# Kernel tuning notes

Hardware: AMD Instinct MI355X
Metric: run time of the kernel (lower is better)

## Reference

```python
import jax, jax.numpy as jnp
import numpy as np

D_MODEL, H, D_FF = 1024, 16, 4096
D_K = D_MODEL // H

def _linear_params(key, fan_in, fan_out):
    kw, kb = jax.random.split(key)
    lim = 1.0 / np.sqrt(fan_in)
    W = jax.random.uniform(kw, (fan_in, fan_out), minval=-lim, maxval=lim, dtype=jnp.float32)
    b = jax.random.uniform(kb, (fan_out,), minval=-lim, maxval=lim, dtype=jnp.float32)
    return W, b

def setup_inputs() -> dict:
    key = jax.random.key(0)
    ks = jax.random.split(key, 8)
    x = jax.random.normal(ks[0], (4, 2048, D_MODEL), dtype=jnp.float32)
    Wq, bq = _linear_params(ks[1], D_MODEL, D_MODEL)
    Wk, bk = _linear_params(ks[2], D_MODEL, D_MODEL)
    Wv, bv = _linear_params(ks[3], D_MODEL, D_MODEL)
    Wo, bo = _linear_params(ks[4], D_MODEL, D_MODEL)
    W1, b1 = _linear_params(ks[5], D_MODEL, D_FF)
    W2, b2 = _linear_params(ks[6], D_FF, D_MODEL)
    g1 = jnp.ones((D_MODEL,), jnp.float32); be1 = jnp.zeros((D_MODEL,), jnp.float32)
    g2 = jnp.ones((D_MODEL,), jnp.float32); be2 = jnp.zeros((D_MODEL,), jnp.float32)
    return {"x": x, "Wq": Wq, "bq": bq, "Wk": Wk, "bk": bk, "Wv": Wv, "bv": bv,
            "Wo": Wo, "bo": bo, "W1": W1, "b1": b1, "W2": W2, "b2": b2,
            "g1": g1, "be1": be1, "g2": g2, "be2": be2}

def _layernorm(x, g, b, eps=1e-5):
    mu = jnp.mean(x, axis=-1, keepdims=True)
    var = jnp.mean(jnp.square(x - mu), axis=-1, keepdims=True)
    return (x - mu) * jax.lax.rsqrt(var + eps) * g + b

def reference(x, Wq, bq, Wk, bk, Wv, bv, Wo, bo, W1, b1, W2, b2, g1, be1, g2, be2):
    B, S, _ = x.shape
    # project and split heads: [B, H, S, D_K]
    q = (x @ Wq + bq).reshape(B, S, H, D_K).transpose(0, 2, 1, 3)
    k = (x @ Wk + bk).reshape(B, S, H, D_K).transpose(0, 2, 1, 3)
    v = (x @ Wv + bv).reshape(B, S, H, D_K).transpose(0, 2, 1, 3)
    scores = jnp.einsum('bhqd,bhkd->bhqk', q, k) / np.sqrt(D_K).astype(np.float32)
    attn = jax.nn.softmax(scores, axis=-1)
    out = jnp.einsum('bhqk,bhkd->bhqd', attn, v)
    out = out.transpose(0, 2, 1, 3).reshape(B, S, D_MODEL)
    attn_out = out @ Wo + bo
    x1 = _layernorm(x + attn_out, g1, be1)
    ffn = jax.nn.relu(x1 @ W1 + b1) @ W2 + b2  # dropout is identity in eval
    return _layernorm(x1 + ffn, g2, be2)
```

## Files before the change

kernel.cpp:

```cpp
#include <hip/hip_runtime.h>

typedef __bf16 bf16;
typedef __bf16 bf16x4 __attribute__((ext_vector_type(4)));
typedef __bf16 bf16x8 __attribute__((ext_vector_type(8)));
typedef float  f32x4  __attribute__((ext_vector_type(4)));

#define DM   1024
#define NH   16
#define DKH  64
#define DFF  4096
#define SEQL 2048
#define NTOK 8192

typedef __attribute__((address_space(1))) void GAS;
typedef __attribute__((address_space(3))) void LAS;

__device__ inline void gload_lds16(const void* g, void* l) {
    __builtin_amdgcn_global_load_lds((GAS*)g, (LAS*)l, 16, 0, 0);
}

__global__ void cast_f32_bf16(const float* __restrict__ in, bf16* __restrict__ out, long n) {
    long i = ((long)blockIdx.x * 256 + threadIdx.x) * 4;
    long stride = (long)gridDim.x * 256 * 4;
    for (; i < n; i += stride) {
        float4 v = *(const float4*)(in + i);
        bf16x4 o = {(bf16)v.x, (bf16)v.y, (bf16)v.z, (bf16)v.w};
        *(bf16x4*)(out + i) = o;
    }
}

__global__ void transpose_cast(const float* __restrict__ src, bf16* __restrict__ dst, int R, int C) {
    __shared__ float t[32][33];
    int c0 = blockIdx.x * 32, r0 = blockIdx.y * 32;
    int tx = threadIdx.x, ty = threadIdx.y;
#pragma unroll
    for (int i = 0; i < 4; ++i)
        t[ty + i * 8][tx] = src[(long)(r0 + ty + i * 8) * C + c0 + tx];
    __syncthreads();
#pragma unroll
    for (int i = 0; i < 4; ++i)
        dst[(long)(c0 + ty + i * 8) * R + r0 + tx] = (bf16)t[tx][ty + i * 8];
}

__global__ void concat3(const float* __restrict__ a, const float* __restrict__ b,
                        const float* __restrict__ c, float* __restrict__ out) {
    int i = blockIdx.x * 256 + threadIdx.x;
    if (i < 1024) out[i] = a[i];
    else if (i < 2048) out[i] = b[i - 1024];
    else if (i < 3072) out[i] = c[i - 2048];
}

__global__ void build_vt(const bf16* __restrict__ qkv, bf16* __restrict__ vt) {
    __shared__ bf16 t[32][33];
    int bh = blockIdx.z, b = bh >> 4, h = bh & 15;
    int s0 = blockIdx.x * 32, d0 = blockIdx.y * 32;
    int tx = threadIdx.x, ty = threadIdx.y;
#pragma unroll
    for (int i = 0; i < 4; ++i)
        t[ty + i * 8][tx] = qkv[(long)(b * SEQL + s0 + ty + i * 8) * 3072 + 2 * DM + h * DKH + d0 + tx];
    __syncthreads();
#pragma unroll
    for (int i = 0; i < 4; ++i)
        vt[((long)bh * DKH + d0 + ty + i * 8) * SEQL + s0 + tx] = (bf16)t[tx][ty + i * 8];
}

__global__ __launch_bounds__(512, 2)
void gemm8p(const bf16* __restrict__ A, const bf16* __restrict__ Bt,
            const float* __restrict__ bias,
            float* __restrict__ Cf, bf16* __restrict__ Ch,
            int N, int lda, int Klen, int relu, long strideCf) {
    __shared__ bf16 As[4][4][256][8];
    __shared__ bf16 Bs[4][4][256][8];
    const int tid = threadIdx.x;
    const int lane = tid & 63;
    const int wv = tid >> 6;
    const int wr = wv >> 2, wc = wv & 3;
    const int lr = lane & 15, lg = lane >> 4;

    unsigned gx = gridDim.x, gy = gridDim.y;
    unsigned nwg = gx * gy * gridDim.z;
    unsigned wg = (blockIdx.z * gy + blockIdx.y) * gx + blockIdx.x;
    unsigned swz = (wg & 7) * (nwg >> 3) + (wg >> 3);
    unsigned bxi = swz % gx;
    unsigned rem = swz / gx;
    unsigned byi = rem % gy, bzi = rem / gy;

    const long brow = (long)byi * 256;
    const long bcol = (long)bxi * 256;
    const bf16* Ap = A + (long)bzi * Klen;
    const bf16* Bp = Bt + (long)bzi * Klen;
    float* Cfp = Cf ? Cf + (long)bzi * strideCf : nullptr;
    const float* biasp = (bzi == 0) ? bias : nullptr;

    auto stageA = [&](int X) {
        const int kt = X * 32, buf = X & 3;
#pragma unroll
        for (int j = 0; j < 2; ++j) {
            int l = j * 512 + tid;
            int kg = l >> 8, row = l & 255;
            gload_lds16(Ap + (brow + row) * (long)lda + kt + kg * 8, &As[buf][kg][row][0]);
        }
    };
    auto stageB = [&](int X) {
        const int kt = X * 32, buf = X & 3;
#pragma unroll
        for (int j = 0; j < 2; ++j) {
            int l = j * 512 + tid;
            int kg = l >> 8, row = l & 255;
            gload_lds16(Bp + (bcol + row) * (long)lda + kt + kg * 8, &Bs[buf][kg][row][0]);
        }
    };

    const int NT = Klen / 32;
    f32x4 acc[8][4] = {};

    for (int p = 0; p < 3 && p < NT; ++p) { stageA(p); stageB(p); }

    for (int T = 0; T < NT; ++T) {
        const int cur = T & 3;
        if (T + 3 < NT) stageA(T + 3);
        if (T + 3 < NT)      asm volatile("s_waitcnt vmcnt(10)" ::: "memory");
        else if (T + 2 < NT) asm volatile("s_waitcnt vmcnt(8)"  ::: "memory");
        else if (T + 1 < NT) asm volatile("s_waitcnt vmcnt(4)"  ::: "memory");
        else                 asm volatile("s_waitcnt vmcnt(0)"  ::: "memory");
        __builtin_amdgcn_s_barrier();
        asm volatile("" ::: "memory");

        bf16x8 bfv[4], af[4];
#pragma unroll
        for (int n = 0; n < 4; ++n)
            bfv[n] = *(const bf16x8*)(&Bs[cur][lg][wc * 64 + n * 16 + lr][0]);
#pragma unroll
        for (int m = 0; m < 4; ++m)
            af[m] = *(const bf16x8*)(&As[cur][lg][wr * 128 + m * 16 + lr][0]);
        asm volatile("s_waitcnt lgkmcnt(0)" ::: "memory");
        __builtin_amdgcn_sched_barrier(0);
        __builtin_amdgcn_s_setprio(1);
#pragma unroll
        for (int m = 0; m < 4; ++m)
#pragma unroll
            for (int n = 0; n < 4; ++n)
                acc[m][n] = __builtin_amdgcn_mfma_f32_16x16x32_bf16(af[m], bfv[n], acc[m][n], 0, 0, 0);
        __builtin_amdgcn_s_setprio(0);

        bf16x8 af2[4];
#pragma unroll
        for (int m = 0; m < 4; ++m)
            af2[m] = *(const bf16x8*)(&As[cur][lg][wr * 128 + (4 + m) * 16 + lr][0]);
        if (T + 3 < NT) stageB(T + 3);
        asm volatile("" ::: "memory");
        __builtin_amdgcn_s_barrier();
        asm volatile("s_waitcnt lgkmcnt(0)" ::: "memory");
        __builtin_amdgcn_sched_barrier(0);
        __builtin_amdgcn_s_setprio(1);
#pragma unroll
        for (int m = 0; m < 4; ++m)
#pragma unroll
            for (int n = 0; n < 4; ++n)
                acc[4 + m][n] = __builtin_amdgcn_mfma_f32_16x16x32_bf16(af2[m], bfv[n], acc[4 + m][n], 0, 0, 0);
        __builtin_amdgcn_s_setprio(0);
        asm volatile("" ::: "memory");
        __builtin_amdgcn_s_barrier();
    }

#pragma unroll
    for (int m = 0; m < 8; ++m) {
#pragma unroll
        for (int n = 0; n < 4; ++n) {
            long gcol = bcol + wc * 64 + n * 16 + lr;
            float bv = biasp ? biasp[gcol] : 0.f;
#pragma unroll
            for (int r = 0; r < 4; ++r) {
                long grow = brow + wr * 128 + m * 16 + lg * 4 + r;
                float v = acc[m][n][r] + bv;
                if (relu) v = v > 0.f ? v : 0.f;
                if (Cfp) Cfp[grow * N + gcol] = v;
                if (Ch) Ch[grow * N + gcol] = (bf16)v;
            }
        }
    }
}

__global__ __launch_bounds__(256, 3)
void attn_fwd(const bf16* __restrict__ qkv, const bf16* __restrict__ vt,
              bf16* __restrict__ attn_o) {
    __shared__ bf16 Ks[2][64][64];
    __shared__ bf16 Vs[2][64][64];
    __shared__ bf16 Plds[4][16][64];
    const int tid = threadIdx.x, lane = tid & 63, w = tid >> 6;
    const int lr = lane & 15, lg = lane >> 4;

    unsigned nwg = gridDim.x * gridDim.y;
    unsigned wg = blockIdx.y * gridDim.x + blockIdx.x;
    unsigned cpx = nwg >> 3;
    unsigned swzid = (wg & 7) * cpx + (wg >> 3);
    const int bx = swzid % gridDim.x, bh = swzid / gridDim.x;
    const int b = bh >> 4, h = bh & 15;
    const int q0 = bx * 128 + w * 32;

    const bf16* Q  = qkv + (long)b * SEQL * 3072 + h * DKH;
    const bf16* Kp = qkv + (long)b * SEQL * 3072 + DM + h * DKH;
    const bf16* Vp = vt + (long)bh * DKH * SEQL;

    const int r0 = w * 8 + (lane >> 3);
    const int cbb = ((lane & 7) * 16) ^ ((r0 & 7) << 4);
    const int cb = cbb >> 1;

    auto stage = [&](int buf, int j0) {
#pragma unroll
        for (int c = 0; c < 2; ++c) {
            bf16* kd = &Ks[buf][0][0] + c * 2048 + w * 512 + lane * 8;
            bf16* vd = &Vs[buf][0][0] + c * 2048 + w * 512 + lane * 8;
            gload_lds16(Kp + (long)(j0 + c * 32 + r0) * 3072 + cb, kd);
            gload_lds16(Vp + (long)(c * 32 + r0) * SEQL + j0 + cb, vd);
        }
    };

    stage(0, 0);

    bf16x8 aq[2][2];
#pragma unroll
    for (int a = 0; a < 2; ++a)
#pragma unroll
        for (int kh = 0; kh < 2; ++kh) {
            bf16x8 q = *(const bf16x8*)(Q + (long)(q0 + a * 16 + lr) * 3072 + kh * 32 + lg * 8);
#pragma unroll
            for (int e = 0; e < 8; ++e) q[e] = (bf16)((float)q[e] * 0.125f);
            aq[a][kh] = q;
        }

    float mrow[2] = {-1e30f, -1e30f};
    float lrow[2] = {0.f, 0.f};
    f32x4 accO[2][4] = {};
    char* pbase = (char*)&Plds[w][0][0];
    const int psw = (lr & 7) << 4;
    const f32x4 zero = {0.f, 0.f, 0.f, 0.f};
    int cur = 0;

    for (int it = 0; it < SEQL / 64; ++it) {
        if (it < SEQL / 64 - 1) {
            stage(cur ^ 1, (it + 1) * 64);
            asm volatile("s_waitcnt vmcnt(4)" ::: "memory");
        } else {
            asm volatile("s_waitcnt vmcnt(0)" ::: "memory");
        }
        __builtin_amdgcn_s_barrier();
        asm volatile("" ::: "memory");

        const char* Kbuf = (const char*)&Ks[cur][0][0];
        const char* Vbuf = (const char*)&Vs[cur][0][0];

        bf16x8 kf[4][2];
#pragma unroll
        for (int jh = 0; jh < 4; ++jh) {
            int row = jh * 16 + lr;
            int sw = (row & 7) << 4;
            kf[jh][0] = *(const bf16x8*)(Kbuf + row * 128 + ((lg * 16) ^ sw));
            kf[jh][1] = *(const bf16x8*)(Kbuf + row * 128 + ((64 + lg * 16) ^ sw));
        }
        bf16x8 vf[4][2];
#pragma unroll
        for (int c = 0; c < 4; ++c) {
            int row = c * 16 + lr;
            int sw = (row & 7) << 4;
            vf[c][0] = *(const bf16x8*)(Vbuf + row * 128 + ((lg * 16) ^ sw));
            vf[c][1] = *(const bf16x8*)(Vbuf + row * 128 + ((64 + lg * 16) ^ sw));
        }

#pragma unroll
        for (int a = 0; a < 2; ++a) {
            f32x4 s[4];
#pragma unroll
            for (int jh = 0; jh < 4; ++jh) {
                f32x4 t = __builtin_amdgcn_mfma_f32_16x16x32_bf16(kf[jh][0], aq[a][0], zero, 0, 0, 0);
                s[jh] = __builtin_amdgcn_mfma_f32_16x16x32_bf16(kf[jh][1], aq[a][1], t, 0, 0, 0);
            }
            float pm = s[0][0];
#pragma unroll
            for (int jh = 0; jh < 4; ++jh)
#pragma unroll
                for (int r = 0; r < 4; ++r) pm = fmaxf(pm, s[jh][r]);
            pm = fmaxf(pm, __shfl_xor(pm, 16));
            pm = fmaxf(pm, __shfl_xor(pm, 32));
            float mnew = fmaxf(mrow[a], pm);
            float al = __expf(mrow[a] - mnew);
            mrow[a] = mnew;
            float psum = 0.f;
#pragma unroll
            for (int jh = 0; jh < 4; ++jh)
#pragma unroll
                for (int r = 0; r < 4; ++r) {
                    float p = __expf(s[jh][r] - mnew);
                    s[jh][r] = p;
                    psum += p;
                }
            psum += __shfl_xor(psum, 16);
            psum += __shfl_xor(psum, 32);
            lrow[a] = lrow[a] * al + psum;
#pragma unroll
            for (int jh = 0; jh < 4; ++jh) {
                bf16x4 pw = {(bf16)s[jh][0], (bf16)s[jh][1], (bf16)s[jh][2], (bf16)s[jh][3]};
                *(bf16x4*)(pbase + lr * 128 + ((jh * 32 + lg * 8) ^ psw)) = pw;
            }
            float alr[4];
#pragma unroll
            for (int r = 0; r < 4; ++r)
                alr[r] = __shfl(al, (lane & 48) | (lg * 4 + r));
#pragma unroll
            for (int c = 0; c < 4; ++c)
#pragma unroll
                for (int r = 0; r < 4; ++r) accO[a][c][r] *= alr[r];
            bf16x8 pa[2];
#pragma unroll
            for (int i = 0; i < 2; ++i)
                pa[i] = *(const bf16x8*)(pbase + lr * 128 + ((i * 64 + lg * 16) ^ psw));
#pragma unroll
            for (int c = 0; c < 4; ++c) {
                accO[a][c] = __builtin_amdgcn_mfma_f32_16x16x32_bf16(pa[0], vf[c][0], accO[a][c], 0, 0, 0);
                accO[a][c] = __builtin_amdgcn_mfma_f32_16x16x32_bf16(pa[1], vf[c][1], accO[a][c], 0, 0, 0);
            }
        }
        asm volatile("" ::: "memory");
        __builtin_amdgcn_s_barrier();
        cur ^= 1;
    }

#pragma unroll
    for (int a = 0; a < 2; ++a) {
        float linv = 1.0f / lrow[a];
        float invr[4];
#pragma unroll
        for (int r = 0; r < 4; ++r)
            invr[r] = __shfl(linv, (lane & 48) | (lg * 4 + r));
#pragma unroll
        for (int r = 0; r < 4; ++r) {
            long grow = (long)b * SEQL + q0 + a * 16 + lg * 4 + r;
#pragma unroll
            for (int c = 0; c < 4; ++c)
                attn_o[grow * DM + h * DKH + c * 16 + lr] = (bf16)(accO[a][c][r] * invr[r]);
        }
    }
}

__global__ __launch_bounds__(256)
void add_ln(const float* __restrict__ A, const float* __restrict__ B,
            const float* __restrict__ B2,
            const float* __restrict__ g, const float* __restrict__ be,
            float* __restrict__ outf, bf16* __restrict__ outh) {
    const int w = threadIdx.x >> 6, lane = threadIdx.x & 63;
    const long row = (long)blockIdx.x * 4 + w;
    const float4* pa = (const float4*)(A + row * DM);
    const float4* pb = (const float4*)(B + row * DM);
    const float4* pb2 = B2 ? (const float4*)(B2 + row * DM) : nullptr;
    float4 v[4];
    float s = 0.f;
#pragma unroll
    for (int i = 0; i < 4; ++i) {
        float4 a = pa[i * 64 + lane], bb = pb[i * 64 + lane];
        v[i] = make_float4(a.x + bb.x, a.y + bb.y, a.z + bb.z, a.w + bb.w);
        if (pb2) {
            float4 b2 = pb2[i * 64 + lane];
            v[i].x += b2.x; v[i].y += b2.y; v[i].z += b2.z; v[i].w += b2.w;
        }
        s += v[i].x + v[i].y + v[i].z + v[i].w;
    }
#pragma unroll
    for (int off = 32; off; off >>= 1) s += __shfl_xor(s, off);
    float mu = s * (1.0f / 1024.0f);
    float var = 0.f;
#pragma unroll
    for (int i = 0; i < 4; ++i) {
        float dx = v[i].x - mu, dy = v[i].y - mu, dz = v[i].z - mu, dw = v[i].w - mu;
        var += dx * dx + dy * dy + dz * dz + dw * dw;
    }
#pragma unroll
    for (int off = 32; off; off >>= 1) var += __shfl_xor(var, off);
    float rs = 1.0f / sqrtf(var * (1.0f / 1024.0f) + 1e-5f);
    const float4* pg = (const float4*)g;
    const float4* pe = (const float4*)be;
#pragma unroll
    for (int i = 0; i < 4; ++i) {
        float4 gg = pg[i * 64 + lane], ee = pe[i * 64 + lane];
        float4 o = make_float4((v[i].x - mu) * rs * gg.x + ee.x,
                               (v[i].y - mu) * rs * gg.y + ee.y,
                               (v[i].z - mu) * rs * gg.z + ee.z,
                               (v[i].w - mu) * rs * gg.w + ee.w);
        if (outf) ((float4*)(outf + row * DM))[i * 64 + lane] = o;
        if (outh) {
            bf16x4 ho = {(bf16)o.x, (bf16)o.y, (bf16)o.z, (bf16)o.w};
            *(bf16x4*)(outh + row * DM + (i * 64 + lane) * 4) = ho;
        }
    }
}

extern "C" void kernel_launch(void* const* d_in, const int* in_sizes, int n_in,
                              void* d_out, int out_size, void* d_ws, size_t ws_size,
                              hipStream_t stream) {
    const float* x   = (const float*)d_in[0];
    const float* Wq  = (const float*)d_in[1];
    const float* bq  = (const float*)d_in[2];
    const float* Wk  = (const float*)d_in[3];
    const float* bk  = (const float*)d_in[4];
    const float* Wv  = (const float*)d_in[5];
    const float* bv  = (const float*)d_in[6];
    const float* Wo  = (const float*)d_in[7];
    const float* bo  = (const float*)d_in[8];
    const float* W1  = (const float*)d_in[9];
    const float* b1  = (const float*)d_in[10];
    const float* W2  = (const float*)d_in[11];
    const float* b2  = (const float*)d_in[12];
    const float* g1  = (const float*)d_in[13];
    const float* be1 = (const float*)d_in[14];
    const float* g2  = (const float*)d_in[15];
    const float* be2 = (const float*)d_in[16];
    float* out = (float*)d_out;

    char* ws = (char*)d_ws;
    size_t off = 0;
    auto alloc = [&](size_t bytes) {
        void* p = ws + off;
        off += (bytes + 255) & ~(size_t)255;
        return p;
    };
    bf16* xh    = (bf16*)alloc((size_t)NTOK * DM * 2);
    bf16* wqkvt = (bf16*)alloc((size_t)3072 * 1024 * 2);
    bf16* wot   = (bf16*)alloc((size_t)1024 * 1024 * 2);
    bf16* w1t   = (bf16*)alloc((size_t)4096 * 1024 * 2);
    bf16* w2t   = (bf16*)alloc((size_t)1024 * 4096 * 2);
    float* bqkv = (float*)alloc((size_t)3072 * 4);
    bf16* qkv   = (bf16*)alloc((size_t)NTOK * 3072 * 2);
    bf16* vtb   = (bf16*)alloc((size_t)NTOK * DM * 2);
    bf16* attno = (bf16*)alloc((size_t)NTOK * DM * 2);
    float* projf  = (float*)alloc((size_t)NTOK * DM * 4);
    float* projf1 = (float*)alloc((size_t)NTOK * DM * 4);
    float* x1f  = (float*)alloc((size_t)NTOK * DM * 4);
    bf16* x1h   = (bf16*)alloc((size_t)NTOK * DM * 2);
    bf16* ffh   = (bf16*)qkv;

    dim3 tb(32, 8);
    cast_f32_bf16<<<2048, 256, 0, stream>>>(x, xh, (long)NTOK * DM);
    transpose_cast<<<dim3(32, 32), tb, 0, stream>>>(Wq, wqkvt, 1024, 1024);
    transpose_cast<<<dim3(32, 32), tb, 0, stream>>>(Wk, wqkvt + (size_t)1024 * 1024, 1024, 1024);
    transpose_cast<<<dim3(32, 32), tb, 0, stream>>>(Wv, wqkvt + (size_t)2048 * 1024, 1024, 1024);
    transpose_cast<<<dim3(32, 32), tb, 0, stream>>>(Wo, wot, 1024, 1024);
    transpose_cast<<<dim3(128, 32), tb, 0, stream>>>(W1, w1t, 1024, 4096);
    transpose_cast<<<dim3(32, 128), tb, 0, stream>>>(W2, w2t, 4096, 1024);
    concat3<<<12, 256, 0, stream>>>(bq, bk, bv, bqkv);

    gemm8p<<<dim3(3072 / 256, 8192 / 256, 1), 512, 0, stream>>>(
        xh, wqkvt, bqkv, nullptr, qkv, 3072, 1024, 1024, 0, 0);
    build_vt<<<dim3(SEQL / 32, 2, 64), tb, 0, stream>>>(qkv, vtb);
    attn_fwd<<<dim3(SEQL / 128, 64), 256, 0, stream>>>(qkv, vtb, attno);
    gemm8p<<<dim3(1024 / 256, 8192 / 256, 2), 512, 0, stream>>>(
        attno, wot, bo, projf, nullptr, 1024, 1024, 512, 0, (long)NTOK * DM);
    add_ln<<<NTOK / 4, 256, 0, stream>>>(x, projf, projf1, g1, be1, x1f, x1h);
    gemm8p<<<dim3(4096 / 256, 8192 / 256, 1), 512, 0, stream>>>(
        x1h, w1t, b1, nullptr, ffh, 4096, 1024, 1024, 1, 0);
    gemm8p<<<dim3(1024 / 256, 8192 / 256, 2), 512, 0, stream>>>(
        ffh, w2t, b2, projf, nullptr, 1024, 4096, 2048, 0, (long)NTOK * DM);
    add_ln<<<NTOK / 4, 256, 0, stream>>>(x1f, projf, projf1, g2, be2, out, nullptr);
}
```

Before: 565.9 us.

## Restructure GEMM to double-buffered K=64 tiles with four-phase MFMA schedule

Replaces the 4-stage, K=32 LDS pipeline in the bf16 GEMM with a 2-stage, K=64 pipeline. Each iteration now splits its MFMA work into four quadrant phases, with LDS fragment reads and next-tile global-to-LDS loads interleaved between barriers. The aim is fewer loop iterations and barriers per unit of K, and more MFMA work per LDS load. In exchange, prefetch depth drops to one tile, a full vmcnt(0) wait ends every iteration, and there are more barriers per iteration.

```diff
diff --git a/kernel.cpp b/kernel.cpp
--- a/kernel.cpp
+++ b/kernel.cpp
@@ -65,12 +65,12 @@
 }
 
 __global__ __launch_bounds__(512, 2)
-void gemm8p(const bf16* __restrict__ A, const bf16* __restrict__ Bt,
+void gemm4p(const bf16* __restrict__ A, const bf16* __restrict__ Bt,
             const float* __restrict__ bias,
             float* __restrict__ Cf, bf16* __restrict__ Ch,
             int N, int lda, int Klen, int relu, long strideCf) {
-    __shared__ bf16 As[4][4][256][8];
-    __shared__ bf16 Bs[4][4][256][8];
+    __shared__ bf16 As[2][8][256][8];
+    __shared__ bf16 Bs[2][8][256][8];
     const int tid = threadIdx.x;
     const int lane = tid & 63;
     const int wv = tid >> 6;
@@ -82,8 +82,8 @@
     unsigned wg = (blockIdx.z * gy + blockIdx.y) * gx + blockIdx.x;
     unsigned swz = (wg & 7) * (nwg >> 3) + (wg >> 3);
     unsigned bxi = swz % gx;
-    unsigned rem = swz / gx;
-    unsigned byi = rem % gy, bzi = rem / gy;
+    unsigned rem2 = swz / gx;
+    unsigned byi = rem2 % gy, bzi = rem2 / gy;
 
     const long brow = (long)byi * 256;
     const long bcol = (long)bxi * 256;
@@ -93,61 +93,67 @@
     const float* biasp = (bzi == 0) ? bias : nullptr;
 
     auto stageA = [&](int X) {
-        const int kt = X * 32, buf = X & 3;
-#pragma unroll
-        for (int j = 0; j < 2; ++j) {
+        const int kt = X * 64, buf = X & 1;
+#pragma unroll
+        for (int j = 0; j < 4; ++j) {
             int l = j * 512 + tid;
             int kg = l >> 8, row = l & 255;
             gload_lds16(Ap + (brow + row) * (long)lda + kt + kg * 8, &As[buf][kg][row][0]);
         }
     };
     auto stageB = [&](int X) {
-        const int kt = X * 32, buf = X & 3;
-#pragma unroll
-        for (int j = 0; j < 2; ++j) {
+        const int kt = X * 64, buf = X & 1;
+#pragma unroll
+        for (int j = 0; j < 4; ++j) {
             int l = j * 512 + tid;
             int kg = l >> 8, row = l & 255;
             gload_lds16(Bp + (bcol + row) * (long)lda + kt + kg * 8, &Bs[buf][kg][row][0]);
         }
     };
 
-    const int NT = Klen / 32;
+    const int NT = Klen / 64;
     f32x4 acc[8][4] = {};
 
-    for (int p = 0; p < 3 && p < NT; ++p) { stageA(p); stageB(p); }
+    stageA(0); stageB(0);
+    asm volatile("s_waitcnt vmcnt(0)" ::: "memory");
+    __builtin_amdgcn_s_barrier();
+    asm volatile("" ::: "memory");
 
     for (int T = 0; T < NT; ++T) {
-        const int cur = T & 3;
-        if (T + 3 < NT) stageA(T + 3);
-        if (T + 3 < NT)      asm volatile("s_waitcnt vmcnt(10)" ::: "memory");
-        else if (T + 2 < NT) asm volatile("s_waitcnt vmcnt(8)"  ::: "memory");
-        else if (T + 1 < NT) asm volatile("s_waitcnt vmcnt(4)"  ::: "memory");
-        else                 asm volatile("s_waitcnt vmcnt(0)"  ::: "memory");
-        __builtin_amdgcn_s_barrier();
-        asm volatile("" ::: "memory");
-
-        bf16x8 bfv[4], af[4];
-#pragma unroll
-        for (int n = 0; n < 4; ++n)
-            bfv[n] = *(const bf16x8*)(&Bs[cur][lg][wc * 64 + n * 16 + lr][0]);
-#pragma unroll
-        for (int m = 0; m < 4; ++m)
-            af[m] = *(const bf16x8*)(&As[cur][lg][wr * 128 + m * 16 + lr][0]);
+        const int cur = T & 1;
+        bf16x8 aL[8], aH[8], bv[8];
+#pragma unroll
+        for (int m = 0; m < 4; ++m) {
+            aL[m * 2]     = *(const bf16x8*)(&As[cur][lg][wr * 128 + m * 16 + lr][0]);
+            aL[m * 2 + 1] = *(const bf16x8*)(&As[cur][4 + lg][wr * 128 + m * 16 + lr][0]);
+        }
+#pragma unroll
+        for (int n = 0; n < 2; ++n) {
+            bv[n * 2]     = *(const bf16x8*)(&Bs[cur][lg][wc * 64 + n * 16 + lr][0]);
+            bv[n * 2 + 1] = *(const bf16x8*)(&Bs[cur][4 + lg][wc * 64 + n * 16 + lr][0]);
+        }
+        if (T + 1 < NT) stageA(T + 1);
+        asm volatile("" ::: "memory");
+        __builtin_amdgcn_s_barrier();
         asm volatile("s_waitcnt lgkmcnt(0)" ::: "memory");
         __builtin_amdgcn_sched_barrier(0);
         __builtin_amdgcn_s_setprio(1);
 #pragma unroll
         for (int m = 0; m < 4; ++m)
 #pragma unroll
-            for (int n = 0; n < 4; ++n)
-                acc[m][n] = __builtin_amdgcn_mfma_f32_16x16x32_bf16(af[m], bfv[n], acc[m][n], 0, 0, 0);
+            for (int n = 0; n < 2; ++n) {
+                acc[m][n] = __builtin_amdgcn_mfma_f32_16x16x32_bf16(aL[m * 2], bv[n * 2], acc[m][n], 0, 0, 0);
+                acc[m][n] = __builtin_amdgcn_mfma_f32_16x16x32_bf16(aL[m * 2 + 1], bv[n * 2 + 1], acc[m][n], 0, 0, 0);
+            }
         __builtin_amdgcn_s_setprio(0);
-
-        bf16x8 af2[4];
-#pragma unroll
-        for (int m = 0; m < 4; ++m)
-            af2[m] = *(const bf16x8*)(&As[cur][lg][wr * 128 + (4 + m) * 16 + lr][0]);
-        if (T + 3 < NT) stageB(T + 3);
+        asm volatile("" ::: "memory");
+        __builtin_amdgcn_s_barrier();
+#pragma unroll
+        for (int n = 2; n < 4; ++n) {
+            bv[n * 2]     = *(const bf16x8*)(&Bs[cur][lg][wc * 64 + n * 16 + lr][0]);
+            bv[n * 2 + 1] = *(const bf16x8*)(&Bs[cur][4 + lg][wc * 64 + n * 16 + lr][0]);
+        }
+        if (T + 1 < NT) stageB(T + 1);
         asm volatile("" ::: "memory");
         __builtin_amdgcn_s_barrier();
         asm volatile("s_waitcnt lgkmcnt(0)" ::: "memory");
@@ -156,9 +162,43 @@
 #pragma unroll
         for (int m = 0; m < 4; ++m)
 #pragma unroll
-            for (int n = 0; n < 4; ++n)
-                acc[4 + m][n] = __builtin_amdgcn_mfma_f32_16x16x32_bf16(af2[m], bfv[n], acc[4 + m][n], 0, 0, 0);
+            for (int n = 2; n < 4; ++n) {
+                acc[m][n] = __builtin_amdgcn_mfma_f32_16x16x32_bf16(aL[m * 2], bv[n * 2], acc[m][n], 0, 0, 0);
+                acc[m][n] = __builtin_amdgcn_mfma_f32_16x16x32_bf16(aL[m * 2 + 1], bv[n * 2 + 1], acc[m][n], 0, 0, 0);
+            }
         __builtin_amdgcn_s_setprio(0);
+        asm volatile("" ::: "memory");
+        __builtin_amdgcn_s_barrier();
+#pragma unroll
+        for (int m = 0; m < 4; ++m) {
+            aH[m * 2]     = *(const bf16x8*)(&As[cur][lg][wr * 128 + (4 + m) * 16 + lr][0]);
+            aH[m * 2 + 1] = *(const bf16x8*)(&As[cur][4 + lg][wr * 128 + (4 + m) * 16 + lr][0]);
+        }
+        asm volatile("" ::: "memory");
+        __builtin_amdgcn_s_barrier();
+        asm volatile("s_waitcnt lgkmcnt(0)" ::: "memory");
+        __builtin_amdgcn_sched_barrier(0);
+        __builtin_amdgcn_s_setprio(1);
+#pragma unroll
+        for (int m = 0; m < 4; ++m)
+#pragma unroll
+            for (int n = 0; n < 2; ++n) {
+                acc[4 + m][n] = __builtin_amdgcn_mfma_f32_16x16x32_bf16(aH[m * 2], bv[n * 2], acc[4 + m][n], 0, 0, 0);
+                acc[4 + m][n] = __builtin_amdgcn_mfma_f32_16x16x32_bf16(aH[m * 2 + 1], bv[n * 2 + 1], acc[4 + m][n], 0, 0, 0);
+            }
+        __builtin_amdgcn_s_setprio(0);
+        asm volatile("" ::: "memory");
+        __builtin_amdgcn_s_barrier();
+        __builtin_amdgcn_s_setprio(1);
+#pragma unroll
+        for (int m = 0; m < 4; ++m)
+#pragma unroll
+            for (int n = 2; n < 4; ++n) {
+                acc[4 + m][n] = __builtin_amdgcn_mfma_f32_16x16x32_bf16(aH[m * 2], bv[n * 2], acc[4 + m][n], 0, 0, 0);
+                acc[4 + m][n] = __builtin_amdgcn_mfma_f32_16x16x32_bf16(aH[m * 2 + 1], bv[n * 2 + 1], acc[4 + m][n], 0, 0, 0);
+            }
+        __builtin_amdgcn_s_setprio(0);
+        if (T + 1 < NT) asm volatile("s_waitcnt vmcnt(0)" ::: "memory");
         asm volatile("" ::: "memory");
         __builtin_amdgcn_s_barrier();
     }
@@ -168,11 +208,11 @@
 #pragma unroll
         for (int n = 0; n < 4; ++n) {
             long gcol = bcol + wc * 64 + n * 16 + lr;
-            float bv = biasp ? biasp[gcol] : 0.f;
+            float bvl = biasp ? biasp[gcol] : 0.f;
 #pragma unroll
             for (int r = 0; r < 4; ++r) {
                 long grow = brow + wr * 128 + m * 16 + lg * 4 + r;
-                float v = acc[m][n][r] + bv;
+                float v = acc[m][n][r] + bvl;
                 if (relu) v = v > 0.f ? v : 0.f;
                 if (Cfp) Cfp[grow * N + gcol] = v;
                 if (Ch) Ch[grow * N + gcol] = (bf16)v;
@@ -447,16 +487,16 @@
     transpose_cast<<<dim3(32, 128), tb, 0, stream>>>(W2, w2t, 4096, 1024);
     concat3<<<12, 256, 0, stream>>>(bq, bk, bv, bqkv);
 
-    gemm8p<<<dim3(3072 / 256, 8192 / 256, 1), 512, 0, stream>>>(
+    gemm4p<<<dim3(3072 / 256, 8192 / 256, 1), 512, 0, stream>>>(
         xh, wqkvt, bqkv, nullptr, qkv, 3072, 1024, 1024, 0, 0);
     build_vt<<<dim3(SEQL / 32, 2, 64), tb, 0, stream>>>(qkv, vtb);
     attn_fwd<<<dim3(SEQL / 128, 64), 256, 0, stream>>>(qkv, vtb, attno);
-    gemm8p<<<dim3(1024 / 256, 8192 / 256, 2), 512, 0, stream>>>(
+    gemm4p<<<dim3(1024 / 256, 8192 / 256, 2), 512, 0, stream>>>(
         attno, wot, bo, projf, nullptr, 1024, 1024, 512, 0, (long)NTOK * DM);
     add_ln<<<NTOK / 4, 256, 0, stream>>>(x, projf, projf1, g1, be1, x1f, x1h);
-    gemm8p<<<dim3(4096 / 256, 8192 / 256, 1), 512, 0, stream>>>(
+    gemm4p<<<dim3(4096 / 256, 8192 / 256, 1), 512, 0, stream>>>(
         x1h, w1t, b1, nullptr, ffh, 4096, 1024, 1024, 1, 0);
-    gemm8p<<<dim3(1024 / 256, 8192 / 256, 2), 512, 0, stream>>>(
+    gemm4p<<<dim3(1024 / 256, 8192 / 256, 2), 512, 0, stream>>>(
         ffh, w2t, b2, projf, nullptr, 1024, 4096, 2048, 0, (long)NTOK * DM);
     add_ln<<<NTOK / 4, 256, 0, stream>>>(x1f, projf, projf1, g2, be2, out, nullptr);
 }
```

After: 611.5 us. 8.1% more time.
